# Performance work log

Measured on AMD Instinct MI355X. Metric: run time of the kernel, lower is better.

Reference implementation:

```python
import jax, jax.numpy as jnp
import numpy as np

B, N, IN_DIM = 64, 4096, 128
D = 128          # slot_size
S = 7            # num_slots
ITERS = 3
HID = 256        # mlp_hdim
EPS = 1e-8       # renorm epsilon
LN_EPS = 1e-5    # torch LayerNorm default


def _ln(x, g, b):
    m = jnp.mean(x, axis=-1, keepdims=True)
    v = jnp.mean((x - m) ** 2, axis=-1, keepdims=True)
    return (x - m) * jax.lax.rsqrt(v + LN_EPS) * g + b


def setup_inputs() -> dict:
    key = jax.random.key(0)
    ks = jax.random.split(key, 16)
    s = 0.02
    return {
        "x": jax.random.normal(ks[0], (B, N, IN_DIM), jnp.float32),
        "noise": jax.random.normal(ks[1], (B, S, D), jnp.float32),
        "Wq": jax.random.normal(ks[2], (D, D), jnp.float32) * s,
        "Wk": jax.random.normal(ks[3], (D, IN_DIM), jnp.float32) * s,
        "Wv": jax.random.normal(ks[4], (D, IN_DIM), jnp.float32) * s,
        "ln_in_g": jnp.ones((IN_DIM,), jnp.float32),
        "ln_in_b": jnp.zeros((IN_DIM,), jnp.float32),
        "ln_slots_g": jnp.ones((D,), jnp.float32),
        "ln_slots_b": jnp.zeros((D,), jnp.float32),
        "ln_mlp_g": jnp.ones((D,), jnp.float32),
        "ln_mlp_b": jnp.zeros((D,), jnp.float32),
        "W_ih": jax.random.normal(ks[5], (3 * D, D), jnp.float32) * s,
        "W_hh": jax.random.normal(ks[6], (3 * D, D), jnp.float32) * s,
        "b_ih": jnp.zeros((3 * D,), jnp.float32),
        "b_hh": jnp.zeros((3 * D,), jnp.float32),
        "W1": jax.random.normal(ks[7], (HID, D), jnp.float32) * s,
        "b1": jnp.zeros((HID,), jnp.float32),
        "W2": jax.random.normal(ks[8], (D, HID), jnp.float32) * s,
        "b2": jnp.zeros((D,), jnp.float32),
        "mu": jax.random.normal(ks[9], (1, 1, D), jnp.float32) * s,
        "logsigma": jax.random.normal(ks[10], (1, D), jnp.float32) * s,
    }


def reference(x, noise, Wq, Wk, Wv, ln_in_g, ln_in_b, ln_slots_g, ln_slots_b,
              ln_mlp_g, ln_mlp_b, W_ih, W_hh, b_ih, b_hh, W1, b1, W2, b2,
              mu, logsigma):
    xn = _ln(x, ln_in_g, ln_in_b)              # (B,N,IN)
    k = xn @ Wk.T                              # (B,N,D)
    v = xn @ Wv.T                              # (B,N,D)

    scale = jax.nn.softplus(logsigma)[None] + 1e-5   # (1,1,D)
    slots = mu + scale * noise                 # rsample, (B,S,D)

    def gru(u, h):
        gx = u @ W_ih.T + b_ih                 # (B*S, 3D)
        gh = h @ W_hh.T + b_hh
        xr, xz, xn_ = jnp.split(gx, 3, axis=-1)
        hr, hz, hn = jnp.split(gh, 3, axis=-1)
        r = jax.nn.sigmoid(xr + hr)
        z = jax.nn.sigmoid(xz + hz)
        n = jnp.tanh(xn_ + r * hn)
        return (1.0 - z) * n + z * h

    inv_sqrt_d = D ** -0.5
    for _ in range(ITERS):
        slots_prev = slots
        sn = _ln(slots, ln_slots_g, ln_slots_b)
        q = sn @ Wq.T                          # (B,S,D)
        scores = inv_sqrt_d * jnp.einsum('bnd,bsd->bns', k, q)
        attn = jax.nn.softmax(scores, axis=-1)           # over slots
        attn = attn + EPS
        attn = attn / jnp.sum(attn, axis=1, keepdims=True)  # renorm over inputs
        updates = jnp.einsum('bns,bnd->bsd', attn, v)    # (B,S,D)
        h = gru(updates.reshape(-1, D), slots_prev.reshape(-1, D))
        slots = h.reshape(x.shape[0], S, D)
        slots = _ln(slots, ln_mlp_g, ln_mlp_b)
        slots = slots + (jax.nn.relu(slots @ W1.T + b1) @ W2.T + b2)
    return slots
```

## Files before the change

kernel.cpp:

```cpp
#include <hip/hip_runtime.h>
#include <hip/hip_bf16.h>
#include <stdint.h>

#define B_ 64
#define N_ 4096
#define D_ 128
#define S_ 7
#define EPS_ 1e-8f
#define LN_EPS_ 1e-5f
#define SC_INV 0.08838834764831843f

typedef float  f32x4  __attribute__((ext_vector_type(4)));
typedef __bf16 bf16x8 __attribute__((ext_vector_type(8)));

#define WIH_OFF 0
#define WHH_OFF 49152
#define W1_OFF  98304
#define W2_OFF  131072
#define WQ_OFF  163840
#define WKT_OFF 180224
#define WV_OFF  196608
#define WBF_TOT 212992

__device__ __forceinline__ uint16_t f2bfbits(float f) {
    uint32_t x = __float_as_uint(f);
    return (uint16_t)((x + 0x7fffu + ((x >> 16) & 1u)) >> 16);
}
__device__ __forceinline__ uint32_t pk2(float a, float b) {
    return (uint32_t)f2bfbits(a) | ((uint32_t)f2bfbits(b) << 16);
}

__global__ __launch_bounds__(256) void k_prep_xn(
    const float* __restrict__ x, const float* __restrict__ lng,
    const float* __restrict__ lnb, uint16_t* __restrict__ xn) {
    const int t = threadIdx.x, wv = t >> 6, lane = t & 63;
    const int lm = lane & 15, hi = lane >> 4;
    const long row = (long)blockIdx.x * 64 + wv * 16 + lm;
    const long ntile = (long)blockIdx.x * 4 + wv;
    const float* xp = x + row * 128 + hi * 8;
    f32x4 xa[4][2];
    #pragma unroll
    for (int k0 = 0; k0 < 4; ++k0) {
        xa[k0][0] = *(const f32x4*)(xp + k0 * 32);
        xa[k0][1] = *(const f32x4*)(xp + k0 * 32 + 4);
    }
    float s = 0.f, sq = 0.f;
    #pragma unroll
    for (int k0 = 0; k0 < 4; ++k0)
        #pragma unroll
        for (int c = 0; c < 2; ++c)
            #pragma unroll
            for (int r = 0; r < 4; ++r) { float v = xa[k0][c][r]; s += v; sq += v * v; }
    s  += __shfl_xor(s, 16);  s  += __shfl_xor(s, 32);
    sq += __shfl_xor(sq, 16); sq += __shfl_xor(sq, 32);
    float mean = s * (1.0f / 128.0f);
    float var  = sq * (1.0f / 128.0f) - mean * mean;
    float rs   = rsqrtf(var + LN_EPS_);
    #pragma unroll
    for (int k0 = 0; k0 < 4; ++k0) {
        f32x4 g0 = *(const f32x4*)(lng + k0 * 32 + hi * 8);
        f32x4 g1 = *(const f32x4*)(lng + k0 * 32 + hi * 8 + 4);
        f32x4 b0 = *(const f32x4*)(lnb + k0 * 32 + hi * 8);
        f32x4 b1 = *(const f32x4*)(lnb + k0 * 32 + hi * 8 + 4);
        float v[8];
        #pragma unroll
        for (int r = 0; r < 4; ++r) {
            v[r]     = (xa[k0][0][r] - mean) * rs * g0[r] + b0[r];
            v[4 + r] = (xa[k0][1][r] - mean) * rs * g1[r] + b1[r];
        }
        uint4 st;
        st.x = pk2(v[0], v[1]); st.y = pk2(v[2], v[3]);
        st.z = pk2(v[4], v[5]); st.w = pk2(v[6], v[7]);
        *(uint4*)(xn + (ntile * 4 + k0) * 512 + lane * 8) = st;
    }
}

__global__ __launch_bounds__(256) void k_init(
    const float* __restrict__ noise, const float* __restrict__ Wk,
    const float* __restrict__ mu, const float* __restrict__ logsigma,
    const float* __restrict__ Wq, const float* __restrict__ lsg,
    const float* __restrict__ lsb,
    const float* __restrict__ Wih, const float* __restrict__ Whh,
    const float* __restrict__ W1, const float* __restrict__ W2,
    const float* __restrict__ Wv,
    float* __restrict__ slots, uint16_t* __restrict__ kqbf,
    uint16_t* __restrict__ wbf) {
    const int t = threadIdx.x;
    __shared__ float sn[128], qr[128];
    __shared__ float red[2];
    const int tid = blockIdx.x * 256 + t;
    const int row = blockIdx.x;
    const int b = row / 7, s = row - b * 7;
    bool act = t < 128;
    float v = 0.f;
    if (act) {
        float sc = log1pf(__expf(logsigma[t])) + 1e-5f;
        v = mu[t] + sc * noise[row * 128 + t];
        slots[row * 128 + t] = v;
    }
    float sv = act ? v : 0.f;
    #pragma unroll
    for (int m = 1; m < 64; m <<= 1) sv += __shfl_xor(sv, m);
    if (act && (t & 63) == 0) red[t >> 6] = sv;
    __syncthreads();
    float mean = (red[0] + red[1]) * (1.0f / 128.0f);
    __syncthreads();
    float dv = act ? (v - mean) : 0.f;
    float sq = dv * dv;
    #pragma unroll
    for (int m = 1; m < 64; m <<= 1) sq += __shfl_xor(sq, m);
    if (act && (t & 63) == 0) red[t >> 6] = sq;
    __syncthreads();
    float var = (red[0] + red[1]) * (1.0f / 128.0f);
    if (act) sn[t] = dv * rsqrtf(var + LN_EPS_) * lsg[t] + lsb[t];
    __syncthreads();
    if (act) {
        const float4* wr = (const float4*)(Wq + t * 128);
        float acc = 0.f;
        #pragma unroll 8
        for (int j = 0; j < 32; ++j) {
            float4 w = wr[j];
            float4 s4 = *(const float4*)(sn + 4 * j);
            acc += w.x * s4.x + w.y * s4.y + w.z * s4.z + w.w * s4.w;
        }
        qr[t] = acc;
    }
    __syncthreads();
    if (act) {
        float kq = 0.f;
        #pragma unroll 8
        for (int o = 0; o < 128; ++o) kq += qr[o] * Wk[o * 128 + t];
        int elem = (t >> 5) * 512 + (s + 16 * ((t >> 3) & 3)) * 8 + (t & 7);
        kqbf[b * 2048 + elem] = f2bfbits(kq * SC_INV);
    }
    if (tid < 73728) {
        int bb = tid / 1152, rem = tid - bb * 1152;
        int sp = 7 + (rem >> 7), d = rem & 127;
        int elem = (d >> 5) * 512 + (sp + 16 * ((d >> 3) & 3)) * 8 + (d & 7);
        kqbf[bb * 2048 + elem] = 0;
    }
    for (int e = tid; e < WBF_TOT; e += 448 * 256) {
        const float* W; int C, el, mode = 0;
        if (e < WHH_OFF)      { W = Wih; C = 128; el = e; }
        else if (e < W1_OFF)  { W = Whh; C = 128; el = e - WHH_OFF; }
        else if (e < W2_OFF)  { W = W1;  C = 128; el = e - W1_OFF; }
        else if (e < WQ_OFF)  { W = W2;  C = 256; el = e - W2_OFF; }
        else if (e < WKT_OFF) { W = Wq;  C = 128; el = e - WQ_OFF; }
        else if (e < WV_OFF)  { W = Wk;  C = 128; el = e - WKT_OFF; mode = 1; }
        else                  { W = Wv;  C = 128; el = e - WV_OFF; }
        int tile = el >> 9, within = el & 511;
        int lp = within >> 3, j = within & 7;
        int lm_ = lp & 15, qd_ = lp >> 4;
        float w;
        if (!mode) {
            int ktN = C >> 5, ot = tile / ktN, kt = tile - ot * ktN;
            w = W[(ot * 16 + lm_) * C + kt * 32 + qd_ * 8 + j];
        } else {
            int dt = tile >> 2, kt = tile & 3;
            w = W[(kt * 32 + qd_ * 8 + j) * 128 + dt * 16 + lm_];
        }
        wbf[e] = f2bfbits(w);
    }
}

__global__ __launch_bounds__(256, 4) void k_attn(
    const uint16_t* __restrict__ xn, const uint16_t* __restrict__ kqbf,
    float* __restrict__ upart, float* __restrict__ cpart) {
    __shared__ __align__(16) uint16_t stage[4][32 * 132];
    __shared__ __align__(16) uint16_t als[4][16 * 36];
    __shared__ float bsum[4][8];
    const int t = threadIdx.x, wv = t >> 6, lane = t & 63;
    const int lm = lane & 15, qd = lane >> 4;
    const int b = blockIdx.x >> 4, chunk = blockIdx.x & 15;
    const int ntb = b * 256 + chunk * 16 + wv * 4;
    const int sbase = qd * 4;

    bf16x8 kqf[4];
    #pragma unroll
    for (int k0 = 0; k0 < 4; ++k0)
        kqf[k0] = *(const bf16x8*)(kqbf + b * 2048 + k0 * 512 + lane * 8);

    uint16_t* xw = stage[wv];
    float* prt = (float*)stage[wv];
    uint16_t* aw = als[wv];
    f32x4 uacc[8];
    #pragma unroll
    for (int i = 0; i < 8; ++i) uacc[i] = (f32x4){0.f, 0.f, 0.f, 0.f};
    f32x4 csl = {0.f, 0.f, 0.f, 0.f};

    #pragma unroll
    for (int sub = 0; sub < 2; ++sub) {
        bf16x8 xf[2][4];
        #pragma unroll
        for (int nt = 0; nt < 2; ++nt)
            #pragma unroll
            for (int k0 = 0; k0 < 4; ++k0)
                xf[nt][k0] = *(const bf16x8*)(xn +
                    ((long)(ntb + sub * 2 + nt) * 4 + k0) * 512 + lane * 8);
        #pragma unroll
        for (int nt = 0; nt < 2; ++nt)
            #pragma unroll
            for (int k0 = 0; k0 < 4; ++k0) {
                int base = (nt * 16 + lm) * 132 + k0 * 32 + qd * 8;
                const uint2* src = (const uint2*)&xf[nt][k0];
                *(uint2*)(xw + base)     = src[0];
                *(uint2*)(xw + base + 4) = src[1];
            }
        f32x4 sc[2];
        #pragma unroll
        for (int nt = 0; nt < 2; ++nt) {
            f32x4 acc = {0.f, 0.f, 0.f, 0.f};
            #pragma unroll
            for (int k0 = 0; k0 < 4; ++k0)
                acc = __builtin_amdgcn_mfma_f32_16x16x32_bf16(kqf[k0], xf[nt][k0], acc, 0, 0, 0);
            sc[nt] = acc;
        }
        #pragma unroll
        for (int nt = 0; nt < 2; ++nt) {
            float mx = -1e30f;
            #pragma unroll
            for (int r = 0; r < 4; ++r)
                if (sbase + r < 7) mx = fmaxf(mx, sc[nt][r]);
            mx = fmaxf(mx, __shfl_xor(mx, 16));
            mx = fmaxf(mx, __shfl_xor(mx, 32));
            float e[4], tot = 0.f;
            #pragma unroll
            for (int r = 0; r < 4; ++r) {
                e[r] = (sbase + r < 7) ? __expf(sc[nt][r] - mx) : 0.f;
                tot += e[r];
            }
            tot += __shfl_xor(tot, 16);
            tot += __shfl_xor(tot, 32);
            float inv = 1.0f / tot;
            #pragma unroll
            for (int r = 0; r < 4; ++r) {
                float a_ = (sbase + r < 7) ? e[r] * inv + EPS_ : 0.f;
                csl[r] += a_;
                aw[(sbase + r) * 36 + nt * 16 + lm] = f2bfbits(a_);
            }
        }
        union { uint2 u[2]; bf16x8 v; } cva;
        cva.u[0] = *(const uint2*)(aw + lm * 36 + qd * 8);
        cva.u[1] = *(const uint2*)(aw + lm * 36 + qd * 8 + 4);
        bf16x8 afr = cva.v;
        #pragma unroll
        for (int dt = 0; dt < 8; ++dt) {
            bf16x8 bfr;
            #pragma unroll
            for (int j = 0; j < 8; ++j)
                bfr[j] = ((const __bf16*)xw)[(qd * 8 + j) * 132 + dt * 16 + lm];
            uacc[dt] = __builtin_amdgcn_mfma_f32_16x16x32_bf16(afr, bfr, uacc[dt], 0, 0, 0);
        }
    }
    #pragma unroll
    for (int m = 1; m < 16; m <<= 1) {
        csl[0] += __shfl_xor(csl[0], m);
        csl[1] += __shfl_xor(csl[1], m);
        csl[2] += __shfl_xor(csl[2], m);
        csl[3] += __shfl_xor(csl[3], m);
    }
    if (lm == 0) {
        #pragma unroll
        for (int r = 0; r < 4; ++r) {
            int s = sbase + r;
            if (s < 7) bsum[wv][s] = csl[r];
        }
    }
    #pragma unroll
    for (int dt = 0; dt < 8; ++dt)
        #pragma unroll
        for (int r = 0; r < 4; ++r) {
            int s = sbase + r;
            if (s < 7) prt[s * 132 + dt * 16 + lm] = uacc[dt][r];
        }
    __syncthreads();
    if (t < 128) {
        const float* p0 = (const float*)stage[0];
        const float* p1 = (const float*)stage[1];
        const float* p2 = (const float*)stage[2];
        const float* p3 = (const float*)stage[3];
        #pragma unroll
        for (int s = 0; s < 7; ++s) {
            int o = s * 132 + t;
            upart[((b * 16 + chunk) * 7 + s) * 128 + t] = p0[o] + p1[o] + p2[o] + p3[o];
        }
    }
    if (t < 7)
        cpart[(b * 16 + chunk) * 7 + t] = bsum[0][t] + bsum[1][t] + bsum[2][t] + bsum[3][t];
}

__global__ __launch_bounds__(256) void k_fused(
    const float* __restrict__ upart, const float* __restrict__ cpart,
    float* __restrict__ slots, const uint16_t* __restrict__ wbf,
    const float* __restrict__ bih, const float* __restrict__ bhh,
    const float* __restrict__ gm, const float* __restrict__ bm,
    const float* __restrict__ b1, const float* __restrict__ b2,
    const float* __restrict__ lsg, const float* __restrict__ lsb,
    uint16_t* __restrict__ kqbf, float* __restrict__ dst, int hasq) {
    __shared__ float uf[16][132];
    __shared__ float hf[16][132];
    __shared__ float slf[16][132];
    __shared__ float hidl[16][264];
    __shared__ float glg[7][776];
    __shared__ float csl[7];
    const int b = blockIdx.x;
    const int t = threadIdx.x, wv = t >> 6, lane = t & 63;
    const int lm = lane & 15, qd = lane >> 4;

    if (t < 7) {
        float c = 0.f;
        #pragma unroll
        for (int i = 0; i < 16; ++i) c += cpart[(b * 16 + i) * 7 + t];
        csl[t] = c;
    }
    for (int idx = t; idx < 896; idx += 256) {
        int s = idx >> 7, d = idx & 127;
        float acc = 0.f;
        #pragma unroll
        for (int i = 0; i < 16; ++i) acc += upart[((b * 16 + i) * 7 + s) * 128 + d];
        slf[s][d] = acc;
        hf[s][d] = slots[(b * 7 + s) * 128 + d];
    }
    __syncthreads();

    {
        bf16x8 apb[4];
        #pragma unroll
        for (int k0 = 0; k0 < 4; ++k0)
            #pragma unroll
            for (int j = 0; j < 8; ++j) apb[k0][j] = (__bf16)slf[lm][k0 * 32 + qd * 8 + j];
        #pragma unroll
        for (int i = 0; i < 2; ++i) {
            int dt = wv * 2 + i;
            f32x4 acc = {0.f, 0.f, 0.f, 0.f};
            #pragma unroll
            for (int k0 = 0; k0 < 4; ++k0) {
                bf16x8 bf = *(const bf16x8*)(wbf + WV_OFF + ((dt * 4 + k0) << 9) + lane * 8);
                acc = __builtin_amdgcn_mfma_f32_16x16x32_bf16(apb[k0], bf, acc, 0, 0, 0);
            }
            #pragma unroll
            for (int r = 0; r < 4; ++r) {
                int s = qd * 4 + r;
                if (s < 7) uf[s][dt * 16 + lm] = acc[r] / csl[s];
            }
        }
    }
    __syncthreads();

    bf16x8 au[4], ah[4];
    #pragma unroll
    for (int k0 = 0; k0 < 4; ++k0)
        #pragma unroll
        for (int j = 0; j < 8; ++j) {
            au[k0][j] = (__bf16)uf[lm][k0 * 32 + qd * 8 + j];
            ah[k0][j] = (__bf16)hf[lm][k0 * 32 + qd * 8 + j];
        }
    {
        const int ih = (wv < 2);
        const uint16_t* W = wbf + (ih ? WIH_OFF : WHH_OFF);
        const int base = ih ? 0 : 384;
        const int w2 = wv & 1;
        #pragma unroll
        for (int i = 0; i < 12; ++i) {
            int ot = w2 * 12 + i;
            f32x4 acc = {0.f, 0.f, 0.f, 0.f};
            #pragma unroll
            for (int k0 = 0; k0 < 4; ++k0) {
                bf16x8 bf = *(const bf16x8*)(W + ((ot * 4 + k0) << 9) + lane * 8);
                acc = __builtin_amdgcn_mfma_f32_16x16x32_bf16(ih ? au[k0] : ah[k0], bf, acc, 0, 0, 0);
            }
            #pragma unroll
            for (int r = 0; r < 4; ++r) {
                int s = qd * 4 + r;
                if (s < 7) glg[s][base + ot * 16 + lm] = acc[r];
            }
        }
    }
    __syncthreads();

    for (int idx = t; idx < 896; idx += 256) {
        int s = idx >> 7, d = idx & 127;
        float xr = glg[s][d] + bih[d];
        float xz = glg[s][128 + d] + bih[128 + d];
        float xg = glg[s][256 + d] + bih[256 + d];
        float hr = glg[s][384 + d] + bhh[d];
        float hz = glg[s][512 + d] + bhh[128 + d];
        float hg = glg[s][640 + d] + bhh[256 + d];
        float r = 1.f / (1.f + __expf(-(xr + hr)));
        float z = 1.f / (1.f + __expf(-(xz + hz)));
        float n = tanhf(xg + r * hg);
        uf[s][d] = (1.f - z) * n + z * hf[s][d];
    }
    __syncthreads();

    for (int s = wv; s < 7; s += 4) {
        float a0 = uf[s][2 * lane], a1 = uf[s][2 * lane + 1];
        float sm = a0 + a1, sq = a0 * a0 + a1 * a1;
        #pragma unroll
        for (int m = 1; m < 64; m <<= 1) { sm += __shfl_xor(sm, m); sq += __shfl_xor(sq, m); }
        float mean = sm * (1.0f / 128.0f);
        float var = sq * (1.0f / 128.0f) - mean * mean;
        float rs = rsqrtf(var + LN_EPS_);
        slf[s][2 * lane]     = (a0 - mean) * rs * gm[2 * lane] + bm[2 * lane];
        slf[s][2 * lane + 1] = (a1 - mean) * rs * gm[2 * lane + 1] + bm[2 * lane + 1];
    }
    __syncthreads();

    bf16x8 as_[4];
    #pragma unroll
    for (int k0 = 0; k0 < 4; ++k0)
        #pragma unroll
        for (int j = 0; j < 8; ++j) as_[k0][j] = (__bf16)slf[lm][k0 * 32 + qd * 8 + j];
    #pragma unroll
    for (int i = 0; i < 4; ++i) {
        int ot = wv * 4 + i;
        f32x4 acc = {0.f, 0.f, 0.f, 0.f};
        #pragma unroll
        for (int k0 = 0; k0 < 4; ++k0) {
            bf16x8 bf = *(const bf16x8*)(wbf + W1_OFF + ((ot * 4 + k0) << 9) + lane * 8);
            acc = __builtin_amdgcn_mfma_f32_16x16x32_bf16(as_[k0], bf, acc, 0, 0, 0);
        }
        #pragma unroll
        for (int r = 0; r < 4; ++r) {
            int s = qd * 4 + r;
            if (s < 7) hidl[s][ot * 16 + lm] = fmaxf(acc[r] + b1[ot * 16 + lm], 0.f);
        }
    }
    __syncthreads();

    bf16x8 ahd[8];
    #pragma unroll
    for (int k0 = 0; k0 < 8; ++k0)
        #pragma unroll
        for (int j = 0; j < 8; ++j) ahd[k0][j] = (__bf16)hidl[lm][k0 * 32 + qd * 8 + j];
    #pragma unroll
    for (int i = 0; i < 2; ++i) {
        int ot = wv * 2 + i;
        f32x4 acc = {0.f, 0.f, 0.f, 0.f};
        #pragma unroll
        for (int k0 = 0; k0 < 8; ++k0) {
            bf16x8 bf = *(const bf16x8*)(wbf + W2_OFF + ((ot * 8 + k0) << 9) + lane * 8);
            acc = __builtin_amdgcn_mfma_f32_16x16x32_bf16(ahd[k0], bf, acc, 0, 0, 0);
        }
        #pragma unroll
        for (int r = 0; r < 4; ++r) {
            int s = qd * 4 + r;
            if (s < 7) {
                float v = slf[s][ot * 16 + lm] + acc[r] + b2[ot * 16 + lm];
                hf[s][ot * 16 + lm] = v;
                dst[(b * 7 + s) * 128 + ot * 16 + lm] = v;
            }
        }
    }
    if (hasq) {
        __syncthreads();
        for (int s = wv; s < 7; s += 4) {
            float a0 = hf[s][2 * lane], a1 = hf[s][2 * lane + 1];
            float sm = a0 + a1, sq = a0 * a0 + a1 * a1;
            #pragma unroll
            for (int m = 1; m < 64; m <<= 1) { sm += __shfl_xor(sm, m); sq += __shfl_xor(sq, m); }
            float mean = sm * (1.0f / 128.0f);
            float var = sq * (1.0f / 128.0f) - mean * mean;
            float rs = rsqrtf(var + LN_EPS_);
            uf[s][2 * lane]     = (a0 - mean) * rs * lsg[2 * lane] + lsb[2 * lane];
            uf[s][2 * lane + 1] = (a1 - mean) * rs * lsg[2 * lane + 1] + lsb[2 * lane + 1];
        }
        __syncthreads();
        bf16x8 an[4];
        #pragma unroll
        for (int k0 = 0; k0 < 4; ++k0)
            #pragma unroll
            for (int j = 0; j < 8; ++j) an[k0][j] = (__bf16)uf[lm][k0 * 32 + qd * 8 + j];
        #pragma unroll
        for (int i = 0; i < 2; ++i) {
            int ot = wv * 2 + i;
            f32x4 acc = {0.f, 0.f, 0.f, 0.f};
            #pragma unroll
            for (int k0 = 0; k0 < 4; ++k0) {
                bf16x8 bf = *(const bf16x8*)(wbf + WQ_OFF + ((ot * 4 + k0) << 9) + lane * 8);
                acc = __builtin_amdgcn_mfma_f32_16x16x32_bf16(an[k0], bf, acc, 0, 0, 0);
            }
            #pragma unroll
            for (int r = 0; r < 4; ++r) {
                int s = qd * 4 + r;
                if (s < 7) slf[s][ot * 16 + lm] = acc[r];
            }
        }
        __syncthreads();
        bf16x8 aq[4];
        #pragma unroll
        for (int k0 = 0; k0 < 4; ++k0)
            #pragma unroll
            for (int j = 0; j < 8; ++j) aq[k0][j] = (__bf16)slf[lm][k0 * 32 + qd * 8 + j];
        #pragma unroll
        for (int i = 0; i < 2; ++i) {
            int dt = wv * 2 + i;
            f32x4 acc = {0.f, 0.f, 0.f, 0.f};
            #pragma unroll
            for (int k0 = 0; k0 < 4; ++k0) {
                bf16x8 bf = *(const bf16x8*)(wbf + WKT_OFF + ((dt * 4 + k0) << 9) + lane * 8);
                acc = __builtin_amdgcn_mfma_f32_16x16x32_bf16(aq[k0], bf, acc, 0, 0, 0);
            }
            #pragma unroll
            for (int r = 0; r < 4; ++r) {
                int s = qd * 4 + r;
                if (s < 7) hidl[s][dt * 16 + lm] = acc[r];
            }
        }
        __syncthreads();
        {
            int kt = t >> 6, lp = t & 63;
            int lmp = lp & 15, qdp = lp >> 4;
            uint16_t h[8];
            #pragma unroll
            for (int j = 0; j < 8; ++j)
                h[j] = (lmp < 7) ? f2bfbits(hidl[lmp][kt * 32 + qdp * 8 + j] * SC_INV) : (uint16_t)0;
            uint4 st;
            st.x = (uint32_t)h[0] | ((uint32_t)h[1] << 16);
            st.y = (uint32_t)h[2] | ((uint32_t)h[3] << 16);
            st.z = (uint32_t)h[4] | ((uint32_t)h[5] << 16);
            st.w = (uint32_t)h[6] | ((uint32_t)h[7] << 16);
            *(uint4*)(kqbf + b * 2048 + t * 8) = st;
        }
    }
}

extern "C" void kernel_launch(void* const* d_in, const int* in_sizes, int n_in,
                              void* d_out, int out_size, void* d_ws, size_t ws_size,
                              hipStream_t stream) {
    const float* x    = (const float*)d_in[0];
    const float* nz   = (const float*)d_in[1];
    const float* Wq   = (const float*)d_in[2];
    const float* Wk   = (const float*)d_in[3];
    const float* Wv   = (const float*)d_in[4];
    const float* ling = (const float*)d_in[5];
    const float* linb = (const float*)d_in[6];
    const float* lsg  = (const float*)d_in[7];
    const float* lsb  = (const float*)d_in[8];
    const float* lmg  = (const float*)d_in[9];
    const float* lmb  = (const float*)d_in[10];
    const float* Wih  = (const float*)d_in[11];
    const float* Whh  = (const float*)d_in[12];
    const float* bih  = (const float*)d_in[13];
    const float* bhh  = (const float*)d_in[14];
    const float* W1   = (const float*)d_in[15];
    const float* b1   = (const float*)d_in[16];
    const float* W2   = (const float*)d_in[17];
    const float* b2   = (const float*)d_in[18];
    const float* mu   = (const float*)d_in[19];
    const float* lsig = (const float*)d_in[20];

    char* wsb = (char*)d_ws;
    uint16_t* xn    = (uint16_t*)(wsb);
    uint16_t* wbf   = (uint16_t*)(wsb + (size_t)67108864);
    uint16_t* kqbf  = (uint16_t*)(wsb + (size_t)67534848);
    float*    slots = (float*)  (wsb + (size_t)67796992);
    float*    upart = (float*)  (wsb + (size_t)68026368);
    float*    cpart = (float*)  (wsb + (size_t)71696384);

    k_prep_xn<<<4096, 256, 0, stream>>>(x, ling, linb, xn);
    k_init<<<448, 256, 0, stream>>>(nz, Wk, mu, lsig, Wq, lsg, lsb,
                                    Wih, Whh, W1, W2, Wv, slots, kqbf, wbf);
    for (int it = 0; it < 3; ++it) {
        float* dst = (it == 2) ? (float*)d_out : slots;
        k_attn<<<1024, 256, 0, stream>>>(xn, kqbf, upart, cpart);
        k_fused<<<64, 256, 0, stream>>>(upart, cpart, slots, wbf, bih, bhh,
                                        lmg, lmb, b1, b2, lsg, lsb,
                                        kqbf, dst, (it < 2) ? 1 : 0);
    }
}
```

Before: 362.3 us.

## Fuse input LayerNorm into first attention pass and prefetch xn fragments

Removes the standalone LayerNorm/bf16-convert kernel and folds it into a new first-iteration attention kernel. That kernel reads fp32 x, normalizes it, writes the bf16 xn for later iterations and uses the fragments directly in registers. This saves one read of xn and one kernel launch. The regular attention kernel now loads both sub-tiles of xn up front, so the loads are in flight earlier, at the cost of more registers. The fused kernel uses launch bounds of 3 blocks per unit, so occupancy may drop.

```diff
diff --git a/kernel.cpp b/kernel.cpp
--- a/kernel.cpp
+++ b/kernel.cpp
@@ -28,51 +28,6 @@
 }
 __device__ __forceinline__ uint32_t pk2(float a, float b) {
     return (uint32_t)f2bfbits(a) | ((uint32_t)f2bfbits(b) << 16);
-}
-
-__global__ __launch_bounds__(256) void k_prep_xn(
-    const float* __restrict__ x, const float* __restrict__ lng,
-    const float* __restrict__ lnb, uint16_t* __restrict__ xn) {
-    const int t = threadIdx.x, wv = t >> 6, lane = t & 63;
-    const int lm = lane & 15, hi = lane >> 4;
-    const long row = (long)blockIdx.x * 64 + wv * 16 + lm;
-    const long ntile = (long)blockIdx.x * 4 + wv;
-    const float* xp = x + row * 128 + hi * 8;
-    f32x4 xa[4][2];
-    #pragma unroll
-    for (int k0 = 0; k0 < 4; ++k0) {
-        xa[k0][0] = *(const f32x4*)(xp + k0 * 32);
-        xa[k0][1] = *(const f32x4*)(xp + k0 * 32 + 4);
-    }
-    float s = 0.f, sq = 0.f;
-    #pragma unroll
-    for (int k0 = 0; k0 < 4; ++k0)
-        #pragma unroll
-        for (int c = 0; c < 2; ++c)
-            #pragma unroll
-            for (int r = 0; r < 4; ++r) { float v = xa[k0][c][r]; s += v; sq += v * v; }
-    s  += __shfl_xor(s, 16);  s  += __shfl_xor(s, 32);
-    sq += __shfl_xor(sq, 16); sq += __shfl_xor(sq, 32);
-    float mean = s * (1.0f / 128.0f);
-    float var  = sq * (1.0f / 128.0f) - mean * mean;
-    float rs   = rsqrtf(var + LN_EPS_);
-    #pragma unroll
-    for (int k0 = 0; k0 < 4; ++k0) {
-        f32x4 g0 = *(const f32x4*)(lng + k0 * 32 + hi * 8);
-        f32x4 g1 = *(const f32x4*)(lng + k0 * 32 + hi * 8 + 4);
-        f32x4 b0 = *(const f32x4*)(lnb + k0 * 32 + hi * 8);
-        f32x4 b1 = *(const f32x4*)(lnb + k0 * 32 + hi * 8 + 4);
-        float v[8];
-        #pragma unroll
-        for (int r = 0; r < 4; ++r) {
-            v[r]     = (xa[k0][0][r] - mean) * rs * g0[r] + b0[r];
-            v[4 + r] = (xa[k0][1][r] - mean) * rs * g1[r] + b1[r];
-        }
-        uint4 st;
-        st.x = pk2(v[0], v[1]); st.y = pk2(v[2], v[3]);
-        st.z = pk2(v[4], v[5]); st.w = pk2(v[6], v[7]);
-        *(uint4*)(xn + (ntile * 4 + k0) * 512 + lane * 8) = st;
-    }
 }
 
 __global__ __launch_bounds__(256) void k_init(
@@ -163,6 +118,169 @@
     }
 }
 
+__global__ __launch_bounds__(256, 3) void k_attn_first(
+    const float* __restrict__ x, const float* __restrict__ lng,
+    const float* __restrict__ lnb, uint16_t* __restrict__ xn,
+    const uint16_t* __restrict__ kqbf,
+    float* __restrict__ upart, float* __restrict__ cpart) {
+    __shared__ __align__(16) uint16_t stage[4][32 * 132];
+    __shared__ __align__(16) uint16_t als[4][16 * 36];
+    __shared__ float bsum[4][8];
+    const int t = threadIdx.x, wv = t >> 6, lane = t & 63;
+    const int lm = lane & 15, qd = lane >> 4;
+    const int b = blockIdx.x >> 4, chunk = blockIdx.x & 15;
+    const int ntb = b * 256 + chunk * 16 + wv * 4;
+    const int sbase = qd * 4;
+
+    bf16x8 kqf[4];
+    #pragma unroll
+    for (int k0 = 0; k0 < 4; ++k0)
+        kqf[k0] = *(const bf16x8*)(kqbf + b * 2048 + k0 * 512 + lane * 8);
+
+    uint16_t* xw = stage[wv];
+    float* prt = (float*)stage[wv];
+    uint16_t* aw = als[wv];
+    f32x4 uacc[8];
+    #pragma unroll
+    for (int i = 0; i < 8; ++i) uacc[i] = (f32x4){0.f, 0.f, 0.f, 0.f};
+    f32x4 csl = {0.f, 0.f, 0.f, 0.f};
+
+    #pragma unroll
+    for (int sub = 0; sub < 2; ++sub) {
+        bf16x8 xfs[2][4];
+        #pragma unroll
+        for (int nt = 0; nt < 2; ++nt) {
+            const long tT = ntb + sub * 2 + nt;
+            const float* xp = x + (tT * 16 + lm) * 128 + qd * 8;
+            f32x4 xr[4][2];
+            #pragma unroll
+            for (int k0 = 0; k0 < 4; ++k0) {
+                xr[k0][0] = *(const f32x4*)(xp + k0 * 32);
+                xr[k0][1] = *(const f32x4*)(xp + k0 * 32 + 4);
+            }
+            float s = 0.f, sq = 0.f;
+            #pragma unroll
+            for (int k0 = 0; k0 < 4; ++k0)
+                #pragma unroll
+                for (int c = 0; c < 2; ++c)
+                    #pragma unroll
+                    for (int r = 0; r < 4; ++r) { float v = xr[k0][c][r]; s += v; sq += v * v; }
+            s  += __shfl_xor(s, 16);  s  += __shfl_xor(s, 32);
+            sq += __shfl_xor(sq, 16); sq += __shfl_xor(sq, 32);
+            float mean = s * (1.0f / 128.0f);
+            float var  = sq * (1.0f / 128.0f) - mean * mean;
+            float rs   = rsqrtf(var + LN_EPS_);
+            #pragma unroll
+            for (int k0 = 0; k0 < 4; ++k0) {
+                f32x4 g0 = *(const f32x4*)(lng + k0 * 32 + qd * 8);
+                f32x4 g1 = *(const f32x4*)(lng + k0 * 32 + qd * 8 + 4);
+                f32x4 b0 = *(const f32x4*)(lnb + k0 * 32 + qd * 8);
+                f32x4 b1 = *(const f32x4*)(lnb + k0 * 32 + qd * 8 + 4);
+                float v[8];
+                #pragma unroll
+                for (int r = 0; r < 4; ++r) {
+                    v[r]     = (xr[k0][0][r] - mean) * rs * g0[r] + b0[r];
+                    v[4 + r] = (xr[k0][1][r] - mean) * rs * g1[r] + b1[r];
+                }
+                union { uint4 u; bf16x8 bf; } cv;
+                cv.u.x = pk2(v[0], v[1]); cv.u.y = pk2(v[2], v[3]);
+                cv.u.z = pk2(v[4], v[5]); cv.u.w = pk2(v[6], v[7]);
+                *(uint4*)(xn + (tT * 4 + k0) * 512 + lane * 8) = cv.u;
+                xfs[nt][k0] = cv.bf;
+            }
+        }
+        #pragma unroll
+        for (int nt = 0; nt < 2; ++nt)
+            #pragma unroll
+            for (int k0 = 0; k0 < 4; ++k0) {
+                int base = (nt * 16 + lm) * 132 + k0 * 32 + qd * 8;
+                const uint2* src = (const uint2*)&xfs[nt][k0];
+                *(uint2*)(xw + base)     = src[0];
+                *(uint2*)(xw + base + 4) = src[1];
+            }
+        f32x4 sc[2];
+        #pragma unroll
+        for (int nt = 0; nt < 2; ++nt) {
+            f32x4 acc = {0.f, 0.f, 0.f, 0.f};
+            #pragma unroll
+            for (int k0 = 0; k0 < 4; ++k0)
+                acc = __builtin_amdgcn_mfma_f32_16x16x32_bf16(kqf[k0], xfs[nt][k0], acc, 0, 0, 0);
+            sc[nt] = acc;
+        }
+        #pragma unroll
+        for (int nt = 0; nt < 2; ++nt) {
+            float mx = -1e30f;
+            #pragma unroll
+            for (int r = 0; r < 4; ++r)
+                if (sbase + r < 7) mx = fmaxf(mx, sc[nt][r]);
+            mx = fmaxf(mx, __shfl_xor(mx, 16));
+            mx = fmaxf(mx, __shfl_xor(mx, 32));
+            float e[4], tot = 0.f;
+            #pragma unroll
+            for (int r = 0; r < 4; ++r) {
+                e[r] = (sbase + r < 7) ? __expf(sc[nt][r] - mx) : 0.f;
+                tot += e[r];
+            }
+            tot += __shfl_xor(tot, 16);
+            tot += __shfl_xor(tot, 32);
+            float inv = 1.0f / tot;
+            #pragma unroll
+            for (int r = 0; r < 4; ++r) {
+                float a_ = (sbase + r < 7) ? e[r] * inv + EPS_ : 0.f;
+                csl[r] += a_;
+                aw[(sbase + r) * 36 + nt * 16 + lm] = f2bfbits(a_);
+            }
+        }
+        union { uint2 u[2]; bf16x8 v; } cva;
+        cva.u[0] = *(const uint2*)(aw + lm * 36 + qd * 8);
+        cva.u[1] = *(const uint2*)(aw + lm * 36 + qd * 8 + 4);
+        bf16x8 afr = cva.v;
+        #pragma unroll
+        for (int dt = 0; dt < 8; ++dt) {
+            bf16x8 bfr;
+            #pragma unroll
+            for (int j = 0; j < 8; ++j)
+                bfr[j] = ((const __bf16*)xw)[(qd * 8 + j) * 132 + dt * 16 + lm];
+            uacc[dt] = __builtin_amdgcn_mfma_f32_16x16x32_bf16(afr, bfr, uacc[dt], 0, 0, 0);
+        }
+    }
+    #pragma unroll
+    for (int m = 1; m < 16; m <<= 1) {
+        csl[0] += __shfl_xor(csl[0], m);
+        csl[1] += __shfl_xor(csl[1], m);
+        csl[2] += __shfl_xor(csl[2], m);
+        csl[3] += __shfl_xor(csl[3], m);
+    }
+    if (lm == 0) {
+        #pragma unroll
+        for (int r = 0; r < 4; ++r) {
+            int s = sbase + r;
+            if (s < 7) bsum[wv][s] = csl[r];
+        }
+    }
+    #pragma unroll
+    for (int dt = 0; dt < 8; ++dt)
+        #pragma unroll
+        for (int r = 0; r < 4; ++r) {
+            int s = sbase + r;
+            if (s < 7) prt[s * 132 + dt * 16 + lm] = uacc[dt][r];
+        }
+    __syncthreads();
+    if (t < 128) {
+        const float* p0 = (const float*)stage[0];
+        const float* p1 = (const float*)stage[1];
+        const float* p2 = (const float*)stage[2];
+        const float* p3 = (const float*)stage[3];
+        #pragma unroll
+        for (int s = 0; s < 7; ++s) {
+            int o = s * 132 + t;
+            upart[((b * 16 + chunk) * 7 + s) * 128 + t] = p0[o] + p1[o] + p2[o] + p3[o];
+        }
+    }
+    if (t < 7)
+        cpart[(b * 16 + chunk) * 7 + t] = bsum[0][t] + bsum[1][t] + bsum[2][t] + bsum[3][t];
+}
+
 __global__ __launch_bounds__(256, 4) void k_attn(
     const uint16_t* __restrict__ xn, const uint16_t* __restrict__ kqbf,
     float* __restrict__ upart, float* __restrict__ cpart) {
@@ -180,6 +298,16 @@
     for (int k0 = 0; k0 < 4; ++k0)
         kqf[k0] = *(const bf16x8*)(kqbf + b * 2048 + k0 * 512 + lane * 8);
 
+    bf16x8 xfs[2][2][4];
+    #pragma unroll
+    for (int sub = 0; sub < 2; ++sub)
+        #pragma unroll
+        for (int nt = 0; nt < 2; ++nt)
+            #pragma unroll
+            for (int k0 = 0; k0 < 4; ++k0)
+                xfs[sub][nt][k0] = *(const bf16x8*)(xn +
+                    ((long)(ntb + sub * 2 + nt) * 4 + k0) * 512 + lane * 8);
+
     uint16_t* xw = stage[wv];
     float* prt = (float*)stage[wv];
     uint16_t* aw = als[wv];
@@ -190,19 +318,12 @@
 
     #pragma unroll
     for (int sub = 0; sub < 2; ++sub) {
-        bf16x8 xf[2][4];
         #pragma unroll
         for (int nt = 0; nt < 2; ++nt)
             #pragma unroll
-            for (int k0 = 0; k0 < 4; ++k0)
-                xf[nt][k0] = *(const bf16x8*)(xn +
-                    ((long)(ntb + sub * 2 + nt) * 4 + k0) * 512 + lane * 8);
-        #pragma unroll
-        for (int nt = 0; nt < 2; ++nt)
-            #pragma unroll
             for (int k0 = 0; k0 < 4; ++k0) {
                 int base = (nt * 16 + lm) * 132 + k0 * 32 + qd * 8;
-                const uint2* src = (const uint2*)&xf[nt][k0];
+                const uint2* src = (const uint2*)&xfs[sub][nt][k0];
                 *(uint2*)(xw + base)     = src[0];
                 *(uint2*)(xw + base + 4) = src[1];
             }
@@ -212,7 +333,7 @@
             f32x4 acc = {0.f, 0.f, 0.f, 0.f};
             #pragma unroll
             for (int k0 = 0; k0 < 4; ++k0)
-                acc = __builtin_amdgcn_mfma_f32_16x16x32_bf16(kqf[k0], xf[nt][k0], acc, 0, 0, 0);
+                acc = __builtin_amdgcn_mfma_f32_16x16x32_bf16(kqf[k0], xfs[sub][nt][k0], acc, 0, 0, 0);
             sc[nt] = acc;
         }
         #pragma unroll
@@ -558,12 +679,14 @@
     float*    upart = (float*)  (wsb + (size_t)68026368);
     float*    cpart = (float*)  (wsb + (size_t)71696384);
 
-    k_prep_xn<<<4096, 256, 0, stream>>>(x, ling, linb, xn);
     k_init<<<448, 256, 0, stream>>>(nz, Wk, mu, lsig, Wq, lsg, lsb,
                                     Wih, Whh, W1, W2, Wv, slots, kqbf, wbf);
     for (int it = 0; it < 3; ++it) {
         float* dst = (it == 2) ? (float*)d_out : slots;
-        k_attn<<<1024, 256, 0, stream>>>(xn, kqbf, upart, cpart);
+        if (it == 0)
+            k_attn_first<<<1024, 256, 0, stream>>>(x, ling, linb, xn, kqbf, upart, cpart);
+        else
+            k_attn<<<1024, 256, 0, stream>>>(xn, kqbf, upart, cpart);
         k_fused<<<64, 256, 0, stream>>>(upart, cpart, slots, wbf, bih, bhh,
                                         lmg, lmb, b1, b2, lsg, lsb,
                                         kqbf, dst, (it < 2) ? 1 : 0);
```

After: 402.9 us. +11.2%, slower.
